# Performance work log

Measured on AMD Instinct MI355X. Metric: run time of the kernel, lower is better.

The kernel has to match this reference:

```python
import jax, jax.numpy as jnp
import numpy as np

_CLIP_MIN = 1e-6
_POS_ALPHA = 1e-3
RADIUS = 3
HALF_D = RADIUS * RADIUS  # 9: patch vector length per class
N_FINE, N_MID, N_HIGH = 19, 7, 3
LAMBDA = 0.5
LOSS_WEIGHT = 1.0
IGNORE = 255

_F2M = np.array([0,0,0,1,1,1,2,2,3,3,4,5,5,6,6,6,6,6,6], dtype=np.int64)
_M2H = np.array([0,0,1,1,1,2,2], dtype=np.int64)
_F2H = _M2H[_F2M]


def setup_inputs():
    key = jax.random.key(0)
    k1, k2, k3, k4 = jax.random.split(key, 4)
    B, H, W, D = 4, 512, 512, 256
    return {
        "step": 5000,
        "embedding": jax.random.normal(k1, (B, D, H // 8, W // 8), jnp.float32),
        "cls_score_before": jax.random.normal(k2, (B, N_FINE, H // 8, W // 8), jnp.float32),
        "cls_score": jax.random.normal(k3, (B, N_FINE + N_MID + N_HIGH, H, W), jnp.float32),
        "label": jax.random.randint(k4, (B, H, W), 0, N_FINE),
        "fine_to_mid": jnp.asarray(_F2M),
        "fine_to_high": jnp.asarray(_F2H),
    }


def _maxpool3(x):  # kernel=stride=3, VALID (rmi_pool_way=0)
    return jax.lax.reduce_window(x, -jnp.inf, jax.lax.max, (1, 1, 3, 3), (1, 1, 3, 3), "VALID")


def _map_get_pairs(la, pr, radius=RADIUS):
    b, c, h, w = la.shape
    nh, nw = h - radius + 1, w - radius + 1
    las = [la[:, :, y:y + nh, x:x + nw] for y in range(radius) for x in range(radius)]
    prs = [pr[:, :, y:y + nh, x:x + nw] for y in range(radius) for x in range(radius)]
    la_v = jnp.stack(las, axis=2).reshape(b, c, radius * radius, nh * nw)
    pr_v = jnp.stack(prs, axis=2).reshape(b, c, radius * radius, nh * nw)
    return la_v, pr_v


def _rmi_lower_bound(oh, probs, vmask):
    # oh, probs: [B,C,H,W]; vmask: [B,1,H,W]
    la = _maxpool3(oh * vmask)
    pr = _maxpool3(probs * vmask + _CLIP_MIN)
    la_v, pr_v = _map_get_pairs(la, pr)  # [B,C,half_d,N]
    la_v = jax.lax.stop_gradient(la_v)   # labels are detached in the original
    la_v = la_v - la_v.mean(axis=-1, keepdims=True)
    pr_v = pr_v - pr_v.mean(axis=-1, keepdims=True)
    diag = _POS_ALPHA * jnp.eye(HALF_D, dtype=la_v.dtype)
    pr_cov = jnp.einsum("bcdn,bcen->bcde", pr_v, pr_v) + diag
    la_cov = jnp.einsum("bcdn,bcen->bcde", la_v, la_v)
    la_pr = jnp.einsum("bcdn,bcen->bcde", la_v, pr_v)
    appro = la_cov - la_pr @ jnp.linalg.solve(pr_cov, jnp.swapaxes(la_pr, -1, -2)) + diag
    chol = jnp.linalg.cholesky(appro)
    logdet = 2.0 * jnp.sum(jnp.log(jnp.diagonal(chol, axis1=-2, axis2=-1) + 1e-8), axis=-1)  # [B,C]
    return jnp.sum(logdet.mean(axis=0) / HALF_D)


def _hiera_bce(oh, pos, neg, vmask):
    # positives judged against min-combined probs, negatives against max-combined probs
    loss = -(oh * jnp.log(pos + 1e-8) + (1.0 - oh) * jnp.log(1.0 - neg + 1e-8)) * vmask
    return loss.sum() / (vmask.sum() * oh.shape[1] + 1e-8)


def _forward(cls_score, label, fine_to_mid, fine_to_high):
    probs = jax.nn.sigmoid(cls_score.astype(jnp.float32))
    valid = (label != IGNORE)
    vmask = valid[:, None].astype(jnp.float32)  # [B,1,H,W]
    lf = jnp.where(valid, label, 0)
    lm = fine_to_mid[lf]
    lh = fine_to_high[lf]
    oh_f = jax.nn.one_hot(lf, N_FINE, axis=1, dtype=jnp.float32)
    oh_m = jax.nn.one_hot(lm, N_MID, axis=1, dtype=jnp.float32)
    oh_h = jax.nn.one_hot(lh, N_HIGH, axis=1, dtype=jnp.float32)
    MCMA = probs[:, :N_FINE]
    MCMB = probs[:, N_FINE:N_FINE + N_MID]
    MCMC = probs[:, N_FINE + N_MID:]
    # upward (max) hierarchy consistency
    segf = jax.ops.segment_max(jnp.moveaxis(MCMA, 1, 0), fine_to_mid, num_segments=N_MID)
    MCMB_c = jnp.maximum(jnp.moveaxis(segf, 0, 1), MCMB)
    mid_to_high = jnp.zeros((N_MID,), dtype=fine_to_high.dtype).at[fine_to_mid].set(fine_to_high)
    segm = jax.ops.segment_max(jnp.moveaxis(MCMB_c, 1, 0), mid_to_high, num_segments=N_HIGH)
    MCMC_c = jnp.maximum(jnp.moveaxis(segm, 0, 1), MCMC)
    # downward (min) hierarchy consistency
    MCLA = jnp.minimum(MCMA, MCMB[:, fine_to_mid])
    MCLB_c = jnp.minimum(MCMB, MCMC[:, mid_to_high])
    MCLC_c = MCMC
    total = 0.0
    for oh, pos, neg in ((oh_f, MCLA, MCMA), (oh_m, MCLB_c, MCMB_c), (oh_h, MCLC_c, MCMC_c)):
        bce = _hiera_bce(oh, pos, neg, vmask)
        rmi = _rmi_lower_bound(oh, pos, vmask)
        total = total + LAMBDA * bce + (1.0 - LAMBDA) * rmi
    return LOSS_WEIGHT * total


def reference(step, embedding, cls_score_before, cls_score, label, fine_to_mid, fine_to_high):
    # step / embedding / cls_score_before feed only the triplet branch (not in provided source)
    return _forward(cls_score, label, fine_to_mid, fine_to_high)
```

## Files before the change

kernel.cpp:

```cpp
#include <hip/hip_runtime.h>
#include <math.h>

namespace {
constexpr int NB = 4, NCHT = 29, NF = 19, NM = 7, NHI = 3;
constexpr int HH = 512, WW = 512;
constexpr int PH  = 170;
constexpr int NHW = 168;
constexpr int NS  = NHW * NHW;
constexpr int NBC = NB * NCHT;
constexpr int CROWS = 14;
constexpr int NCH2  = NHW / CROWS;
constexpr int LDSW  = 176;

constexpr int F2M[NF] = {0,0,0,1,1,1,2,2,3,3,4,5,5,6,6,6,6,6,6};
constexpr int M2H[NM] = {0,0,1,1,1,2,2};

constexpr unsigned long long packTbl(const int* a, int n) {
  unsigned long long p = 0;
  for (int i = 0; i < n; i++) p |= (unsigned long long)(a[i]) << (3 * i);
  return p;
}
constexpr int F2H_[NF] = {0,0,0,0,0,0,1,1,1,1,1,2,2,2,2,2,2,2,2};
constexpr unsigned long long PF2M = packTbl(F2M, NF);
constexpr unsigned long long PF2H = packTbl(F2H_, NF);

constexpr int    WS_S1  = 16;
constexpr int    WS_COV = 4096;
constexpr int    WS_RED = 49152;
constexpr size_t PLANEF = (size_t)170 * 11 * NBC * 16;
constexpr size_t WS_LA  = 65536;
constexpr size_t WS_PR  = WS_LA + PLANEF;
constexpr size_t WS_ZERO_BYTES = (size_t)(WS_RED + 64 * 16) * 4;
}

#define GLOAD16(gsrc, ldst)                                                     \
  __builtin_amdgcn_global_load_lds(                                             \
      (const __attribute__((address_space(1))) void*)(gsrc),                    \
      (__attribute__((address_space(3))) void*)(ldst), 16, 0, 0)

template <int W4>
__device__ __forceinline__ void kA_body(
    const int bx, const int wy, const int b, const int tid,
    const float* __restrict__ cls, const int* __restrict__ label,
    float* __restrict__ ws, float* sPixF, unsigned* sMask, float (*sRed)[3]) {
  constexpr int NCOL = 4 * W4;
  constexpr int CST  = 3 * NCOL;
  constexpr int T3   = 3 * W4;
  const int x0   = 48 * bx;
  const int y0   = 3 * wy;
  const int rmax = (wy == 170) ? 1 : 2;

  for (int i = tid; i < NCHT * T3; i += 192) {
    const int c   = i / T3;
    const int rem = i - c * T3;
    const int r   = rem / W4;
    const int f   = rem - r * W4;
    const int rr  = (r <= rmax) ? r : rmax;
    const float* src =
        cls + ((size_t)(b * NCHT + c) * HH + (y0 + rr)) * WW + x0 + 4 * f;
    GLOAD16(src, &sPixF[4 * i]);
  }
  __syncthreads();

  float bce0 = 0.f, bce1 = 0.f, bce2 = 0.f, cnt = 0.f;
  if (tid < CST) {
    const int r = tid / NCOL;
    if (r <= rmax) {
      const int col = tid - r * NCOL;
      const int lbl = label[((size_t)b * HH + (y0 + r)) * WW + x0 + col];
      const bool valid = (lbl != 255);
      const int lf = valid ? lbl : 0;
      const int lm = (int)((PF2M >> (3 * lf)) & 7ull);
      const int lh = (int)((PF2H >> (3 * lf)) & 7ull);
      const float vm = valid ? 1.f : 0.f;

      float x[NCHT];
      #pragma unroll
      for (int c = 0; c < NCHT; c++) x[c] = sPixF[c * CST + tid];

      float segf[NM];
      #pragma unroll
      for (int m = 0; m < NM; m++) segf[m] = -1e30f;
      #pragma unroll
      for (int f = 0; f < NF; f++) segf[F2M[f]] = fmaxf(segf[F2M[f]], x[f]);
      float pBx[NM];
      #pragma unroll
      for (int m = 0; m < NM; m++) pBx[m] = fmaxf(segf[m], x[NF + m]);
      float segm[NHI];
      #pragma unroll
      for (int k = 0; k < NHI; k++) segm[k] = -1e30f;
      #pragma unroll
      for (int m = 0; m < NM; m++) segm[M2H[m]] = fmaxf(segm[M2H[m]], pBx[m]);
      float pCx[NHI];
      #pragma unroll
      for (int k = 0; k < NHI; k++) pCx[k] = fmaxf(segm[k], x[NF + NM + k]);

      float prA = 1.f, prB = 1.f, prM = 1.f, prH = 1.f;
      #pragma unroll
      for (int f = 0; f < NF; f++) {
        const float mx  = fminf(x[f], x[NF + F2M[f]]);
        const float arg = (f == lf) ? -mx : x[f];
        const float t = __builtin_fmaf(vm, __expf(arg), 1.f);
        if (f < 10) prA *= t; else prB *= t;
        sPixF[f * CST + tid] = valid ? mx : -1e30f;
      }
      #pragma unroll
      for (int m = 0; m < NM; m++) {
        const float mx  = fminf(x[NF + m], x[NF + NM + M2H[m]]);
        const float arg = (m == lm) ? -mx : pBx[m];
        prM *= __builtin_fmaf(vm, __expf(arg), 1.f);
        sPixF[(NF + m) * CST + tid] = valid ? mx : -1e30f;
      }
      #pragma unroll
      for (int k = 0; k < NHI; k++) {
        const float px  = x[NF + NM + k];
        const float arg = (k == lh) ? -px : pCx[k];
        prH *= __builtin_fmaf(vm, __expf(arg), 1.f);
        sPixF[(NF + NM + k) * CST + tid] = valid ? px : -1e30f;
      }
      bce0 = __logf(prA) + __logf(prB);
      bce1 = __logf(prM);
      bce2 = __logf(prH);
      sMask[tid] = valid ? ((1u << lf) | (1u << (19 + lm)) | (1u << (26 + lh))) : 0u;
      cnt = vm;
    }
  }

  #pragma unroll
  for (int m = 32; m >= 1; m >>= 1) {
    bce0 += __shfl_xor(bce0, m);
    bce1 += __shfl_xor(bce1, m);
    bce2 += __shfl_xor(bce2, m);
    cnt  += __shfl_xor(cnt, m);
  }
  {
    const int wave = tid >> 6, lane = tid & 63;
    if (lane == 0) {
      sRed[0][wave] = bce0; sRed[1][wave] = bce1;
      sRed[2][wave] = bce2; sRed[3][wave] = cnt;
    }
  }
  __syncthreads();

  if (wy < 170) {
    const size_t base = (size_t)(wy * 11 + bx) * 1856 + (size_t)b * 464;
    float* la = ws + WS_LA + base;
    float* pr = ws + WS_PR + base;
    for (int t = tid; t < 464; t += 192) {
      const int c = t >> 4, w = t & 15;
      const int c0 = 3 * w;
      unsigned m = 0u;
      #pragma unroll
      for (int r = 0; r < 3; r++)
        m |= sMask[r * NCOL + c0] | sMask[r * NCOL + c0 + 1] |
             sMask[r * NCOL + c0 + 2];
      la[t] = (float)((m >> c) & 1u);
      float v = -1e30f;
      #pragma unroll
      for (int r = 0; r < 3; r++)
        v = fmaxf(v, fmaxf(fmaxf(sPixF[c * CST + r * NCOL + c0],
                                 sPixF[c * CST + r * NCOL + c0 + 1]),
                           sPixF[c * CST + r * NCOL + c0 + 2]));
      pr[t] = __builtin_amdgcn_rcpf(1.f + __expf(-v)) + 1e-6f;
    }
  }

  if (tid == 0) {
    const int slot = (bx + 11 * (wy + 171 * b)) & 63;
    float* dst = ws + WS_RED + slot * 16;
    atomicAdd(&dst[0], sRed[0][0] + sRed[0][1] + sRed[0][2]);
    atomicAdd(&dst[1], sRed[1][0] + sRed[1][1] + sRed[1][2]);
    atomicAdd(&dst[2], sRed[2][0] + sRed[2][1] + sRed[2][2]);
    atomicAdd(&dst[3], sRed[3][0] + sRed[3][1] + sRed[3][2]);
  }
}

__global__ __launch_bounds__(192)
void kA(const float* __restrict__ cls, const int* __restrict__ label,
        float* __restrict__ ws) {
  __shared__ __align__(16) float sPixF[NCHT * 144];
  __shared__ unsigned sMask[144];
  __shared__ float    sRed[4][3];
  const int bx = blockIdx.x, wy = blockIdx.y, b = blockIdx.z;
  if (bx < 10)
    kA_body<12>(bx, wy, b, threadIdx.x, cls, label, ws, sPixF, sMask, sRed);
  else
    kA_body<8>(bx, wy, b, threadIdx.x, cls, label, ws, sPixF, sMask, sRed);
}

__global__ __launch_bounds__(192)
void kCov(const float* __restrict__ ws_base, float* __restrict__ cov,
          float* __restrict__ s1out) {
  const int bc    = blockIdx.x / NCH2;
  const int chunk = blockIdx.x % NCH2;
  const int tid   = threadIdx.x;
  const int tile  = tid / 32;
  const int g     = tid % 32;
  const int ta = (tile < 3) ? 0 : ((tile < 5) ? 1 : 2);
  const int tb = (tile < 3) ? tile : ((tile < 5) ? tile - 2 : 2);
  const bool diag = (ta == tb);

  __shared__ __align__(16) float sA[16 * LDSW];
  __shared__ __align__(16) float sP[16 * LDSW];

  const int r0 = chunk * CROWS;
  const float* laG = ws_base + WS_LA;
  const float* prG = ws_base + WS_PR;
  for (int i = tid; i < 16 * 44; i += 192) {
    const int r  = i / 44;
    const int ch = i - 44 * r;
    const int wx = 4 * ch;
    const size_t src =
        (size_t)((r0 + r) * 11 + (wx >> 4)) * 1856 + (size_t)bc * 16 + (wx & 15);
    GLOAD16(laG + src, &sA[4 * i]);
    GLOAD16(prG + src, &sP[4 * i]);
  }
  __syncthreads();

  const float* baseA[6];
  const float* baseB[6];
  #pragma unroll
  for (int k = 0; k < 6; k++) {
    int r = 6 * ta + k, rr = r % 9;
    baseA[k] = ((r < 9) ? sA : sP) + (rr / 3) * LDSW + (rr % 3);
    int r2 = 6 * tb + k, rr2 = r2 % 9;
    baseB[k] = ((r2 < 9) ? sA : sP) + (rr2 / 3) * LDSW + (rr2 % 3);
  }

  float acc[6][6];
  #pragma unroll
  for (int k = 0; k < 6; k++)
    #pragma unroll
    for (int l = 0; l < 6; l++) acc[k][l] = 0.f;
  float sums[6];
  #pragma unroll
  for (int k = 0; k < 6; k++) sums[k] = 0.f;

  for (int lr = 0; lr < CROWS; lr++) {
    const int rowoff = lr * LDSW;
    for (int lc = g; lc < NHW; lc += 32) {
      float va[6], vb[6];
      #pragma unroll
      for (int k = 0; k < 6; k++) va[k] = baseA[k][rowoff + lc];
      #pragma unroll
      for (int k = 0; k < 6; k++) vb[k] = baseB[k][rowoff + lc];
      #pragma unroll
      for (int k = 0; k < 6; k++)
        #pragma unroll
        for (int l = 0; l < 6; l++) acc[k][l] = fmaf(va[k], vb[l], acc[k][l]);
      if (diag) {
        #pragma unroll
        for (int k = 0; k < 6; k++) sums[k] += va[k];
      }
    }
  }

  #pragma unroll
  for (int k = 0; k < 6; k++)
    #pragma unroll
    for (int l = 0; l < 6; l++) {
      float v = acc[k][l];
      #pragma unroll
      for (int m = 16; m >= 1; m >>= 1) v += __shfl_xor(v, m);
      acc[k][l] = v;
    }
  if (diag) {
    #pragma unroll
    for (int k = 0; k < 6; k++) {
      float v = sums[k];
      #pragma unroll
      for (int m = 16; m >= 1; m >>= 1) v += __shfl_xor(v, m);
      sums[k] = v;
    }
  }
  if (g == 0) {
    float* dst = cov + (size_t)bc * 324;
    #pragma unroll
    for (int k = 0; k < 6; k++)
      #pragma unroll
      for (int l = 0; l < 6; l++)
        atomicAdd(&dst[(6 * ta + k) * 18 + 6 * tb + l], acc[k][l]);
    if (diag) {
      #pragma unroll
      for (int k = 0; k < 6; k++)
        atomicAdd(&s1out[bc * 32 + 6 * ta + k], sums[k]);
    }
  }
}

__global__ __launch_bounds__(64)
void kSolve(const float* __restrict__ cov_all, const float* __restrict__ s1,
            float* __restrict__ acc) {
  const int bc   = blockIdx.x;
  const int lane = threadIdx.x;
  const float* cr = cov_all + (size_t)bc * 324;
  const double n = (double)NS;

  double mu[18];
  #pragma unroll
  for (int r = 0; r < 18; r++) mu[r] = (double)s1[bc * 32 + r] / n;
#define CC(i, j) ((double)cr[(i) * 18 + (j)] - n * mu[(i)] * mu[(j)])

  double row[9];
  #pragma unroll
  for (int j = 0; j < 9; j++)
    row[j] = (lane < 9 && j <= lane) ? CC(9 + j, 9 + lane) : 0.0;
  if (lane < 9) row[lane] += 1e-3;

  #pragma unroll
  for (int k = 0; k < 9; k++) {
    if (lane == k) {
      double s = row[k];
      #pragma unroll
      for (int m = 0; m < k; m++) s -= row[m] * row[m];
      row[k] = sqrt(fmax(s, 1e-300));
    }
    double rk[9];
    #pragma unroll
    for (int m = 0; m <= k; m++) rk[m] = __shfl(row[m], k);
    if (lane > k && lane < 9) {
      double s = row[k];
      #pragma unroll
      for (int m = 0; m < k; m++) s -= row[m] * rk[m];
      row[k] = s / rk[k];
    }
  }

  double Lm[9][9];
  #pragma unroll
  for (int i = 0; i < 9; i++)
    #pragma unroll
    for (int m = 0; m <= i; m++) Lm[i][m] = __shfl(row[m], i);

  double mc[9];
  #pragma unroll
  for (int r = 0; r < 9; r++) mc[r] = 0.0;
  if (lane < 9) {
    #pragma unroll
    for (int r = 0; r < 9; r++) {
      double s = CC(lane, 9 + r);
      #pragma unroll
      for (int m = 0; m < r; m++) s -= Lm[r][m] * mc[m];
      mc[r] = s / Lm[r][r];
    }
  }

  double a2[9];
  #pragma unroll
  for (int j = 0; j < 9; j++) a2[j] = 0.0;
  #pragma unroll
  for (int j = 0; j < 9; j++) {
    double mj[9];
    #pragma unroll
    for (int r = 0; r < 9; r++) mj[r] = __shfl(mc[r], j);
    double dot = 0.0;
    #pragma unroll
    for (int r = 0; r < 9; r++) dot += mc[r] * mj[r];
    if (lane < 9 && j <= lane)
      a2[j] = CC(j, lane) - dot + ((j == lane) ? 1e-3 : 0.0);
  }
#undef CC

  double myld = 0.0;
  #pragma unroll
  for (int k = 0; k < 9; k++) {
    if (lane == k) {
      double s = a2[k];
      #pragma unroll
      for (int m = 0; m < k; m++) s -= a2[m] * a2[m];
      double d = sqrt(fmax(s, 0.0));
      a2[k] = d;
      myld = 2.0 * log(d + 1e-8);
    }
    double rk[9];
    #pragma unroll
    for (int m = 0; m <= k; m++) rk[m] = __shfl(a2[m], k);
    if (lane > k && lane < 9) {
      double s = a2[k];
      #pragma unroll
      for (int m = 0; m < k; m++) s -= a2[m] * rk[m];
      a2[k] = s / rk[k];
    }
  }
  #pragma unroll
  for (int m = 32; m >= 1; m >>= 1) myld += __shfl_xor(myld, m);
  if (lane == 0) atomicAdd(&acc[4], (float)myld);
}

__global__ void kFin(const float* __restrict__ ws, float* __restrict__ out) {
  const int tid = threadIdx.x;
  const float* slot = ws + WS_RED + tid * 16;
  float b0 = slot[0], b1 = slot[1], b2 = slot[2], b3 = slot[3];
  #pragma unroll
  for (int m = 32; m >= 1; m >>= 1) {
    b0 += __shfl_xor(b0, m);
    b1 += __shfl_xor(b1, m);
    b2 += __shfl_xor(b2, m);
    b3 += __shfl_xor(b3, m);
  }
  if (tid == 0) {
    const double cnt = (double)b3;
    const double bce = 0.5 * ((double)b0 / (cnt * NF + 1e-8) +
                              (double)b1 / (cnt * NM + 1e-8) +
                              (double)b2 / (cnt * NHI + 1e-8));
    const double rmi = 0.5 * (double)ws[4] / (double)(NB * 9);
    out[0] = (float)(bce + rmi);
  }
}

extern "C" void kernel_launch(void* const* d_in, const int* in_sizes, int n_in,
                              void* d_out, int out_size, void* d_ws, size_t ws_size,
                              hipStream_t stream) {
  (void)in_sizes; (void)n_in; (void)out_size; (void)ws_size;
  const float* cls   = (const float*)d_in[3];
  const int*   label = (const int*)d_in[4];
  float* ws = (float*)d_ws;

  hipMemsetAsync(d_ws, 0, WS_ZERO_BYTES, stream);

  dim3 gA(11, 171, NB);
  kA<<<gA, 192, 0, stream>>>(cls, label, ws);
  kCov<<<NBC * NCH2, 192, 0, stream>>>(ws, ws + WS_COV, ws + WS_S1);
  kSolve<<<NBC, 64, 0, stream>>>(ws + WS_COV, ws + WS_S1, ws);
  kFin<<<1, 64, 0, stream>>>(ws, (float*)d_out);
}
```

Baseline: 117.0 us.

## Batch four (b,c) planes per kCov block with shorter row chunks

kCov now loads a contiguous 64-float span covering four consecutive (b,c) planes for each row and 11-column tile, so its global loads are wider and fully coalesced. Each 256-thread block covers 4 planes × 6 covariance tiles = 24 tile tasks over three passes of eight groups, and rows per chunk drop from 14 to 6, so the grid has 29·28 blocks. The aim is better load coalescing and more blocks for occupancy, paid for with extra halo-row reloads, more atomics per covariance entry, and select-based LDS index arithmetic in the inner loop.

```diff
diff --git a/kernel.cpp b/kernel.cpp
--- a/kernel.cpp
+++ b/kernel.cpp
@@ -8,9 +8,10 @@
 constexpr int NHW = 168;
 constexpr int NS  = NHW * NHW;
 constexpr int NBC = NB * NCHT;
-constexpr int CROWS = 14;
+constexpr int CROWS = 6;
 constexpr int NCH2  = NHW / CROWS;
-constexpr int LDSW  = 176;
+constexpr int ROWS  = CROWS + 2;
+constexpr int LROW  = 11 * 64;
 
 constexpr int F2M[NF] = {0,0,0,1,1,1,2,2,3,3,4,5,5,6,6,6,6,6,6};
 constexpr int M2H[NM] = {0,0,1,1,1,2,2};
@@ -188,102 +189,118 @@
     kA_body<8>(bx, wy, b, threadIdx.x, cls, label, ws, sPixF, sMask, sRed);
 }
 
-__global__ __launch_bounds__(192)
+__global__ __launch_bounds__(256)
 void kCov(const float* __restrict__ ws_base, float* __restrict__ cov,
           float* __restrict__ s1out) {
-  const int bc    = blockIdx.x / NCH2;
+  const int bcg   = blockIdx.x / NCH2;
   const int chunk = blockIdx.x % NCH2;
   const int tid   = threadIdx.x;
-  const int tile  = tid / 32;
-  const int g     = tid % 32;
-  const int ta = (tile < 3) ? 0 : ((tile < 5) ? 1 : 2);
-  const int tb = (tile < 3) ? tile : ((tile < 5) ? tile - 2 : 2);
-  const bool diag = (ta == tb);
-
-  __shared__ __align__(16) float sA[16 * LDSW];
-  __shared__ __align__(16) float sP[16 * LDSW];
+  const int grp   = tid >> 5;
+  const int g     = tid & 31;
+
+  __shared__ __align__(16) float sA[ROWS * LROW];
+  __shared__ __align__(16) float sP[ROWS * LROW];
 
   const int r0 = chunk * CROWS;
   const float* laG = ws_base + WS_LA;
   const float* prG = ws_base + WS_PR;
-  for (int i = tid; i < 16 * 44; i += 192) {
-    const int r  = i / 44;
-    const int ch = i - 44 * r;
-    const int wx = 4 * ch;
+  for (int i = tid; i < ROWS * 176; i += 256) {
+    const int r   = i / 176;
+    const int rem = i - 176 * r;
+    const int bxt = rem >> 4;
+    const int q   = rem & 15;
     const size_t src =
-        (size_t)((r0 + r) * 11 + (wx >> 4)) * 1856 + (size_t)bc * 16 + (wx & 15);
+        (size_t)((r0 + r) * 11 + bxt) * 1856 + (size_t)bcg * 64 + 4 * q;
     GLOAD16(laG + src, &sA[4 * i]);
     GLOAD16(prG + src, &sP[4 * i]);
   }
   __syncthreads();
 
-  const float* baseA[6];
-  const float* baseB[6];
-  #pragma unroll
-  for (int k = 0; k < 6; k++) {
-    int r = 6 * ta + k, rr = r % 9;
-    baseA[k] = ((r < 9) ? sA : sP) + (rr / 3) * LDSW + (rr % 3);
-    int r2 = 6 * tb + k, rr2 = r2 % 9;
-    baseB[k] = ((r2 < 9) ? sA : sP) + (rr2 / 3) * LDSW + (rr2 % 3);
-  }
-
-  float acc[6][6];
-  #pragma unroll
-  for (int k = 0; k < 6; k++)
-    #pragma unroll
-    for (int l = 0; l < 6; l++) acc[k][l] = 0.f;
-  float sums[6];
-  #pragma unroll
-  for (int k = 0; k < 6; k++) sums[k] = 0.f;
-
-  for (int lr = 0; lr < CROWS; lr++) {
-    const int rowoff = lr * LDSW;
-    for (int lc = g; lc < NHW; lc += 32) {
-      float va[6], vb[6];
-      #pragma unroll
-      for (int k = 0; k < 6; k++) va[k] = baseA[k][rowoff + lc];
-      #pragma unroll
-      for (int k = 0; k < 6; k++) vb[k] = baseB[k][rowoff + lc];
+  for (int s = 0; s < 3; s++) {
+    const int tt   = grp + 8 * s;
+    const int j    = tt / 6;
+    const int tile = tt - 6 * j;
+    const int ta = (tile < 3) ? 0 : ((tile < 5) ? 1 : 2);
+    const int tb = (tile < 3) ? tile : ((tile < 5) ? tile - 2 : 2);
+    const bool diag = (ta == tb);
+    const int bc = 4 * bcg + j;
+
+    const float* bA[6]; int cA[6];
+    const float* bB[6]; int cB[6];
+    #pragma unroll
+    for (int k = 0; k < 6; k++) {
+      const int rv = 6 * ta + k, rr = rv % 9;
+      bA[k] = ((rv < 9) ? sA : sP) + (rr / 3) * LROW + j * 16;
+      cA[k] = rr % 3;
+      const int rv2 = 6 * tb + k, rr2 = rv2 % 9;
+      bB[k] = ((rv2 < 9) ? sA : sP) + (rr2 / 3) * LROW + j * 16;
+      cB[k] = rr2 % 3;
+    }
+
+    float acc[6][6];
+    #pragma unroll
+    for (int k = 0; k < 6; k++)
+      #pragma unroll
+      for (int l = 0; l < 6; l++) acc[k][l] = 0.f;
+    float sums[6];
+    #pragma unroll
+    for (int k = 0; k < 6; k++) sums[k] = 0.f;
+
+    for (int lr = 0; lr < CROWS; lr++) {
+      const int rowoff = lr * LROW;
+      for (int lc = g; lc < NHW; lc += 32) {
+        const int w0 = lc,     a0 = ((w0 >> 4) << 6) + (w0 & 15);
+        const int w1 = lc + 1, a1 = ((w1 >> 4) << 6) + (w1 & 15);
+        const int w2 = lc + 2, a2 = ((w2 >> 4) << 6) + (w2 & 15);
+        float va[6], vb[6];
+        #pragma unroll
+        for (int k = 0; k < 6; k++) {
+          const int sa = (cA[k] == 0) ? a0 : ((cA[k] == 1) ? a1 : a2);
+          va[k] = bA[k][rowoff + sa];
+          const int sb = (cB[k] == 0) ? a0 : ((cB[k] == 1) ? a1 : a2);
+          vb[k] = bB[k][rowoff + sb];
+        }
+        #pragma unroll
+        for (int k = 0; k < 6; k++)
+          #pragma unroll
+          for (int l = 0; l < 6; l++) acc[k][l] = fmaf(va[k], vb[l], acc[k][l]);
+        if (diag) {
+          #pragma unroll
+          for (int k = 0; k < 6; k++) sums[k] += va[k];
+        }
+      }
+    }
+
+    #pragma unroll
+    for (int k = 0; k < 6; k++)
+      #pragma unroll
+      for (int l = 0; l < 6; l++) {
+        float v = acc[k][l];
+        #pragma unroll
+        for (int m = 16; m >= 1; m >>= 1) v += __shfl_xor(v, m);
+        acc[k][l] = v;
+      }
+    if (diag) {
+      #pragma unroll
+      for (int k = 0; k < 6; k++) {
+        float v = sums[k];
+        #pragma unroll
+        for (int m = 16; m >= 1; m >>= 1) v += __shfl_xor(v, m);
+        sums[k] = v;
+      }
+    }
+    if (g == 0) {
+      float* dst = cov + (size_t)bc * 324;
       #pragma unroll
       for (int k = 0; k < 6; k++)
         #pragma unroll
-        for (int l = 0; l < 6; l++) acc[k][l] = fmaf(va[k], vb[l], acc[k][l]);
+        for (int l = 0; l < 6; l++)
+          atomicAdd(&dst[(6 * ta + k) * 18 + 6 * tb + l], acc[k][l]);
       if (diag) {
         #pragma unroll
-        for (int k = 0; k < 6; k++) sums[k] += va[k];
-      }
-    }
-  }
-
-  #pragma unroll
-  for (int k = 0; k < 6; k++)
-    #pragma unroll
-    for (int l = 0; l < 6; l++) {
-      float v = acc[k][l];
-      #pragma unroll
-      for (int m = 16; m >= 1; m >>= 1) v += __shfl_xor(v, m);
-      acc[k][l] = v;
-    }
-  if (diag) {
-    #pragma unroll
-    for (int k = 0; k < 6; k++) {
-      float v = sums[k];
-      #pragma unroll
-      for (int m = 16; m >= 1; m >>= 1) v += __shfl_xor(v, m);
-      sums[k] = v;
-    }
-  }
-  if (g == 0) {
-    float* dst = cov + (size_t)bc * 324;
-    #pragma unroll
-    for (int k = 0; k < 6; k++)
-      #pragma unroll
-      for (int l = 0; l < 6; l++)
-        atomicAdd(&dst[(6 * ta + k) * 18 + 6 * tb + l], acc[k][l]);
-    if (diag) {
-      #pragma unroll
-      for (int k = 0; k < 6; k++)
-        atomicAdd(&s1out[bc * 32 + 6 * ta + k], sums[k]);
+        for (int k = 0; k < 6; k++)
+          atomicAdd(&s1out[bc * 32 + 6 * ta + k], sums[k]);
+      }
     }
   }
 }
@@ -420,7 +437,7 @@
 
   dim3 gA(11, 171, NB);
   kA<<<gA, 192, 0, stream>>>(cls, label, ws);
-  kCov<<<NBC * NCH2, 192, 0, stream>>>(ws, ws + WS_COV, ws + WS_S1);
+  kCov<<<29 * NCH2, 256, 0, stream>>>(ws, ws + WS_COV, ws + WS_S1);
   kSolve<<<NBC, 64, 0, stream>>>(ws + WS_COV, ws + WS_S1, ws);
   kFin<<<1, 64, 0, stream>>>(ws, (float*)d_out);
 }
```

After: 164.6 us. +40.7%, slower.

## Restructure covariance kernel with row-major planes, register sliding windows and symmetric accumulation

Applied to the files above, without the earlier changes.

kA now writes the pooled label and probability maps into per-(batch,class) row-major planes. kCov streams rows directly from global memory, builds the 3x3 patch vectors with a register sliding window and lane shuffles instead of LDS staging, and accumulates only the upper triangle of the symmetric 18x18 covariance, split across two half-waves. This is meant to cut LDS traffic and redundant FMAs, at the cost of high register pressure (93 accumulators) and uncoalesced-overlap global loads. It relies on the solver reading only the upper triangle of the diagonal blocks.

```diff
diff --git a/kernel.cpp b/kernel.cpp
--- a/kernel.cpp
+++ b/kernel.cpp
@@ -8,9 +8,8 @@
 constexpr int NHW = 168;
 constexpr int NS  = NHW * NHW;
 constexpr int NBC = NB * NCHT;
-constexpr int CROWS = 14;
-constexpr int NCH2  = NHW / CROWS;
-constexpr int LDSW  = 176;
+constexpr int RSTR = 176;
+constexpr int CCH  = 7;
 
 constexpr int F2M[NF] = {0,0,0,1,1,1,2,2,3,3,4,5,5,6,6,6,6,6,6};
 constexpr int M2H[NM] = {0,0,1,1,1,2,2};
@@ -27,9 +26,9 @@
 constexpr int    WS_S1  = 16;
 constexpr int    WS_COV = 4096;
 constexpr int    WS_RED = 49152;
-constexpr size_t PLANEF = (size_t)170 * 11 * NBC * 16;
+constexpr size_t PLANER = (size_t)NBC * PH * RSTR;
 constexpr size_t WS_LA  = 65536;
-constexpr size_t WS_PR  = WS_LA + PLANEF;
+constexpr size_t WS_PR  = WS_LA + PLANER;
 constexpr size_t WS_ZERO_BYTES = (size_t)(WS_RED + 64 * 16) * 4;
 }
 
@@ -143,9 +142,8 @@
   __syncthreads();
 
   if (wy < 170) {
-    const size_t base = (size_t)(wy * 11 + bx) * 1856 + (size_t)b * 464;
-    float* la = ws + WS_LA + base;
-    float* pr = ws + WS_PR + base;
+    float* laB = ws + WS_LA;
+    float* prB = ws + WS_PR;
     for (int t = tid; t < 464; t += 192) {
       const int c = t >> 4, w = t & 15;
       const int c0 = 3 * w;
@@ -154,14 +152,15 @@
       for (int r = 0; r < 3; r++)
         m |= sMask[r * NCOL + c0] | sMask[r * NCOL + c0 + 1] |
              sMask[r * NCOL + c0 + 2];
-      la[t] = (float)((m >> c) & 1u);
       float v = -1e30f;
       #pragma unroll
       for (int r = 0; r < 3; r++)
         v = fmaxf(v, fmaxf(fmaxf(sPixF[c * CST + r * NCOL + c0],
                                  sPixF[c * CST + r * NCOL + c0 + 1]),
                            sPixF[c * CST + r * NCOL + c0 + 2]));
-      pr[t] = __builtin_amdgcn_rcpf(1.f + __expf(-v)) + 1e-6f;
+      const size_t addr = ((size_t)(b * NCHT + c) * PH + wy) * RSTR + 16 * bx + w;
+      laB[addr] = (float)((m >> c) & 1u);
+      prB[addr] = __builtin_amdgcn_rcpf(1.f + __expf(-v)) + 1e-6f;
     }
   }
 
@@ -188,102 +187,147 @@
     kA_body<8>(bx, wy, b, threadIdx.x, cls, label, ws, sPixF, sMask, sRed);
 }
 
-__global__ __launch_bounds__(192)
+__global__ __launch_bounds__(256, 2)
 void kCov(const float* __restrict__ ws_base, float* __restrict__ cov,
           float* __restrict__ s1out) {
-  const int bc    = blockIdx.x / NCH2;
-  const int chunk = blockIdx.x % NCH2;
+  const int bc    = blockIdx.x;
+  const int chunk = blockIdx.y;
   const int tid   = threadIdx.x;
-  const int tile  = tid / 32;
-  const int g     = tid % 32;
-  const int ta = (tile < 3) ? 0 : ((tile < 5) ? 1 : 2);
-  const int tb = (tile < 3) ? tile : ((tile < 5) ? tile - 2 : 2);
-  const bool diag = (ta == tb);
-
-  __shared__ __align__(16) float sA[16 * LDSW];
-  __shared__ __align__(16) float sP[16 * LDSW];
-
-  const int r0 = chunk * CROWS;
-  const float* laG = ws_base + WS_LA;
-  const float* prG = ws_base + WS_PR;
-  for (int i = tid; i < 16 * 44; i += 192) {
-    const int r  = i / 44;
-    const int ch = i - 44 * r;
-    const int wx = 4 * ch;
-    const size_t src =
-        (size_t)((r0 + r) * 11 + (wx >> 4)) * 1856 + (size_t)bc * 16 + (wx & 15);
-    GLOAD16(laG + src, &sA[4 * i]);
-    GLOAD16(prG + src, &sP[4 * i]);
-  }
-  __syncthreads();
-
-  const float* baseA[6];
-  const float* baseB[6];
-  #pragma unroll
-  for (int k = 0; k < 6; k++) {
-    int r = 6 * ta + k, rr = r % 9;
-    baseA[k] = ((r < 9) ? sA : sP) + (rr / 3) * LDSW + (rr % 3);
-    int r2 = 6 * tb + k, rr2 = r2 % 9;
-    baseB[k] = ((r2 < 9) ? sA : sP) + (rr2 / 3) * LDSW + (rr2 % 3);
-  }
-
-  float acc[6][6];
-  #pragma unroll
-  for (int k = 0; k < 6; k++)
-    #pragma unroll
-    for (int l = 0; l < 6; l++) acc[k][l] = 0.f;
-  float sums[6];
-  #pragma unroll
-  for (int k = 0; k < 6; k++) sums[k] = 0.f;
-
-  for (int lr = 0; lr < CROWS; lr++) {
-    const int rowoff = lr * LDSW;
-    for (int lc = g; lc < NHW; lc += 32) {
-      float va[6], vb[6];
-      #pragma unroll
-      for (int k = 0; k < 6; k++) va[k] = baseA[k][rowoff + lc];
-      #pragma unroll
-      for (int k = 0; k < 6; k++) vb[k] = baseB[k][rowoff + lc];
-      #pragma unroll
-      for (int k = 0; k < 6; k++)
-        #pragma unroll
-        for (int l = 0; l < 6; l++) acc[k][l] = fmaf(va[k], vb[l], acc[k][l]);
-      if (diag) {
-        #pragma unroll
-        for (int k = 0; k < 6; k++) sums[k] += va[k];
+  const int lane  = tid & 63;
+  const int half  = (tid >> 6) & 1;
+  const int rg    = tid >> 7;
+  const int rbase = chunk * 24 + rg * 12;
+
+  const float* laP = ws_base + WS_LA + (size_t)bc * PH * RSTR;
+  const float* prP = ws_base + WS_PR + (size_t)bc * PH * RSTR;
+
+  float acc[93];
+  float sums[9];
+  #pragma unroll
+  for (int k = 0; k < 93; k++) acc[k] = 0.f;
+  #pragma unroll
+  for (int k = 0; k < 9; k++) sums[k] = 0.f;
+
+  for (int cb = 0; cb < 3; cb++) {
+    const int sx  = 62 * cb + lane;
+    const int sxc = (sx < 169) ? sx : 169;
+    const float okf = (lane < 62 && sx < NHW) ? 1.f : 0.f;
+    const float* lc0 = laP + sxc;
+    const float* pc0 = prP + sxc;
+
+    float A[9], P[9];
+    {
+      float x = lc0[(size_t)(rbase + 0) * RSTR];
+      A[0] = x; A[1] = __shfl_down(x, 1); A[2] = __shfl_down(x, 2);
+      x = lc0[(size_t)(rbase + 1) * RSTR];
+      A[3] = x; A[4] = __shfl_down(x, 1); A[5] = __shfl_down(x, 2);
+      x = pc0[(size_t)(rbase + 0) * RSTR];
+      P[0] = x; P[1] = __shfl_down(x, 1); P[2] = __shfl_down(x, 2);
+      x = pc0[(size_t)(rbase + 1) * RSTR];
+      P[3] = x; P[4] = __shfl_down(x, 1); P[5] = __shfl_down(x, 2);
+    }
+    #pragma unroll
+    for (int ii = 0; ii < 12; ii++) {
+      const int r = rbase + ii;
+      {
+        float x = lc0[(size_t)(r + 2) * RSTR];
+        A[6] = x; A[7] = __shfl_down(x, 1); A[8] = __shfl_down(x, 2);
+        x = pc0[(size_t)(r + 2) * RSTR];
+        P[6] = x; P[7] = __shfl_down(x, 1); P[8] = __shfl_down(x, 2);
       }
-    }
-  }
-
-  #pragma unroll
-  for (int k = 0; k < 6; k++)
-    #pragma unroll
-    for (int l = 0; l < 6; l++) {
-      float v = acc[k][l];
-      #pragma unroll
-      for (int m = 16; m >= 1; m >>= 1) v += __shfl_xor(v, m);
-      acc[k][l] = v;
-    }
-  if (diag) {
-    #pragma unroll
-    for (int k = 0; k < 6; k++) {
-      float v = sums[k];
-      #pragma unroll
-      for (int m = 16; m >= 1; m >>= 1) v += __shfl_xor(v, m);
-      sums[k] = v;
-    }
-  }
-  if (g == 0) {
+      float vm[18];
+      #pragma unroll
+      for (int k = 0; k < 9; k++) vm[k] = A[k] * okf;
+      #pragma unroll
+      for (int k = 0; k < 9; k++) vm[9 + k] = P[k] * okf;
+
+      if (half == 0) {
+        int q = 0;
+        #pragma unroll
+        for (int i = 0; i < 6; i++)
+          #pragma unroll
+          for (int j = i; j < 6; j++) { acc[q] = fmaf(vm[i], vm[j], acc[q]); q++; }
+        #pragma unroll
+        for (int i = 0; i < 6; i++)
+          #pragma unroll
+          for (int j = 0; j < 6; j++) { acc[q] = fmaf(vm[i], vm[6 + j], acc[q]); q++; }
+        #pragma unroll
+        for (int i = 0; i < 6; i++)
+          #pragma unroll
+          for (int j = 0; j < 6; j++) { acc[q] = fmaf(vm[i], vm[12 + j], acc[q]); q++; }
+        #pragma unroll
+        for (int k = 0; k < 9; k++) sums[k] += vm[k];
+      } else {
+        int q = 0;
+        #pragma unroll
+        for (int i = 0; i < 6; i++)
+          #pragma unroll
+          for (int j = i; j < 6; j++) { acc[q] = fmaf(vm[6 + i], vm[6 + j], acc[q]); q++; }
+        #pragma unroll
+        for (int i = 0; i < 6; i++)
+          #pragma unroll
+          for (int j = 0; j < 6; j++) { acc[q] = fmaf(vm[6 + i], vm[12 + j], acc[q]); q++; }
+        #pragma unroll
+        for (int i = 0; i < 6; i++)
+          #pragma unroll
+          for (int j = i; j < 6; j++) { acc[q] = fmaf(vm[12 + i], vm[12 + j], acc[q]); q++; }
+        #pragma unroll
+        for (int k = 0; k < 9; k++) sums[k] += vm[9 + k];
+      }
+      #pragma unroll
+      for (int k = 0; k < 6; k++) { A[k] = A[k + 3]; P[k] = P[k + 3]; }
+    }
+  }
+
+  #pragma unroll
+  for (int k = 0; k < 93; k++) {
+    float v = acc[k];
+    #pragma unroll
+    for (int m = 32; m >= 1; m >>= 1) v += __shfl_xor(v, m);
+    acc[k] = v;
+  }
+  #pragma unroll
+  for (int k = 0; k < 9; k++) {
+    float v = sums[k];
+    #pragma unroll
+    for (int m = 32; m >= 1; m >>= 1) v += __shfl_xor(v, m);
+    sums[k] = v;
+  }
+
+  if (lane == 0) {
     float* dst = cov + (size_t)bc * 324;
-    #pragma unroll
-    for (int k = 0; k < 6; k++)
-      #pragma unroll
-      for (int l = 0; l < 6; l++)
-        atomicAdd(&dst[(6 * ta + k) * 18 + 6 * tb + l], acc[k][l]);
-    if (diag) {
-      #pragma unroll
-      for (int k = 0; k < 6; k++)
-        atomicAdd(&s1out[bc * 32 + 6 * ta + k], sums[k]);
+    if (half == 0) {
+      int q = 0;
+      #pragma unroll
+      for (int i = 0; i < 6; i++)
+        #pragma unroll
+        for (int j = i; j < 6; j++) { atomicAdd(&dst[i * 18 + j], acc[q]); q++; }
+      #pragma unroll
+      for (int i = 0; i < 6; i++)
+        #pragma unroll
+        for (int j = 0; j < 6; j++) { atomicAdd(&dst[i * 18 + 6 + j], acc[q]); q++; }
+      #pragma unroll
+      for (int i = 0; i < 6; i++)
+        #pragma unroll
+        for (int j = 0; j < 6; j++) { atomicAdd(&dst[i * 18 + 12 + j], acc[q]); q++; }
+      #pragma unroll
+      for (int k = 0; k < 9; k++) atomicAdd(&s1out[bc * 32 + k], sums[k]);
+    } else {
+      int q = 0;
+      #pragma unroll
+      for (int i = 0; i < 6; i++)
+        #pragma unroll
+        for (int j = i; j < 6; j++) { atomicAdd(&dst[(6 + i) * 18 + 6 + j], acc[q]); q++; }
+      #pragma unroll
+      for (int i = 0; i < 6; i++)
+        #pragma unroll
+        for (int j = 0; j < 6; j++) { atomicAdd(&dst[(6 + i) * 18 + 12 + j], acc[q]); q++; }
+      #pragma unroll
+      for (int i = 0; i < 6; i++)
+        #pragma unroll
+        for (int j = i; j < 6; j++) { atomicAdd(&dst[(12 + i) * 18 + 12 + j], acc[q]); q++; }
+      #pragma unroll
+      for (int k = 0; k < 9; k++) atomicAdd(&s1out[bc * 32 + 9 + k], sums[k]);
     }
   }
 }
@@ -420,7 +464,7 @@
 
   dim3 gA(11, 171, NB);
   kA<<<gA, 192, 0, stream>>>(cls, label, ws);
-  kCov<<<NBC * NCH2, 192, 0, stream>>>(ws, ws + WS_COV, ws + WS_S1);
+  kCov<<<dim3(NBC, CCH), 256, 0, stream>>>(ws, ws + WS_COV, ws + WS_S1);
   kSolve<<<NBC, 64, 0, stream>>>(ws + WS_COV, ws + WS_S1, ws);
   kFin<<<1, 64, 0, stream>>>(ws, (float*)d_out);
 }
```

New measurement: 363.2 us. 3.1x slower.
